# Performance work log

Hardware: AMD Instinct MI355X
Metric: run time of the kernel (lower is better)

## Reference

```python
import jax, jax.numpy as jnp
import numpy as np

EPS = 1e-8

def setup_inputs() -> dict:
    key = jax.random.key(0)
    ks = jax.random.split(key, 4)
    B, N, D = 16, 2048, 1024
    APP = 1024
    x = jax.random.normal(ks[0], (B, N, D), dtype=jnp.float32)
    mask = jax.random.uniform(ks[1], (N, B), dtype=jnp.float32)  # [N, B] per original
    Wp = jax.random.normal(ks[2], (1024, D), dtype=jnp.float32) * 0.02
    bp = jnp.zeros((1024,), dtype=jnp.float32)
    Wv = jax.random.normal(ks[3], (APP, D), dtype=jnp.float32) * 0.02
    bv = jnp.zeros((APP,), dtype=jnp.float32)
    return {"x": x, "mask": mask, "Wp": Wp, "bp": bp, "Wv": Wv, "bv": bv}

def reference(x, mask, Wp, bp, Wv, bv):
    # proj + ReLU: [B,N,1024]
    xp = jax.nn.relu(jnp.einsum('bnd,pd->bnp', x, Wp) + bp)
    # L2-normalize along feature dim (matches xp / (norm + eps))
    xp = xp / (jnp.linalg.norm(xp, axis=2, keepdims=True) + EPS)
    # mask: [N,B] -> [B,N] (transpose+reshape in original yields [B,1,N])
    m = mask.T  # [B, N]
    # att_i = sum_j m_j * <xp_i, xp_j> / sum_j m_j  == <xp_i, sum_j m_j xp_j> / sum_j m_j
    ws = jnp.einsum('bn,bnp->bp', m, xp)                # [B, 1024]
    att = jnp.einsum('bnp,bp->bn', xp, ws) / jnp.sum(m, axis=1, keepdims=True)  # [B, N]
    # value + ReLU: [B,N,APP]
    xv = jax.nn.relu(jnp.einsum('bnd,ad->bna', x, Wv) + bv)
    return att[:, :, None] * xv
```

## Files before the change

### kernel.cpp

```cpp
#include <hip/hip_runtime.h>

#define B_  16
#define N_  2048
#define D_  1024
#define P_  1024
#define M_  (B_*N_)

typedef __attribute__((ext_vector_type(8))) short bf16x8;
typedef __attribute__((ext_vector_type(4))) float f32x4;

__device__ __forceinline__ float bf2f(unsigned short u) {
    union { unsigned int i; float f; } v; v.i = ((unsigned int)u) << 16; return v.f;
}
__device__ __forceinline__ unsigned short f2bf(float f) {
    union { unsigned int i; float f; } v; v.f = f;
    unsigned int i = v.i;
    return (unsigned short)((i + 0x7FFFu + ((i >> 16) & 1u)) >> 16);
}

__device__ __forceinline__ void async_cp16(const void* g, void* s) {
    __builtin_amdgcn_global_load_lds((const __attribute__((address_space(1))) void*)g,
                                     (__attribute__((address_space(3))) void*)s,
                                     16, 0, 0);
}

__global__ void cvt_all_k(const float* __restrict__ x,  unsigned short* __restrict__ xb,
                          const float* __restrict__ Wp, unsigned short* __restrict__ Wpb,
                          const float* __restrict__ Wv, unsigned short* __restrict__ Wvb)
{
    const int stride = gridDim.x * 256 * 4;
    const int base = (blockIdx.x * 256 + threadIdx.x) * 4;
    for (int i = base; i < M_ * D_; i += stride) {
        float4 v = *(const float4*)(x + i);
        union { unsigned short u[4]; unsigned long long ll; } p;
        p.u[0]=f2bf(v.x); p.u[1]=f2bf(v.y); p.u[2]=f2bf(v.z); p.u[3]=f2bf(v.w);
        *(unsigned long long*)(xb + i) = p.ll;
    }
    for (int i = base; i < P_ * D_; i += stride) {
        float4 v = *(const float4*)(Wp + i);
        union { unsigned short u[4]; unsigned long long ll; } p;
        p.u[0]=f2bf(v.x); p.u[1]=f2bf(v.y); p.u[2]=f2bf(v.z); p.u[3]=f2bf(v.w);
        *(unsigned long long*)(Wpb + i) = p.ll;
    }
    for (int i = base; i < P_ * D_; i += stride) {
        float4 v = *(const float4*)(Wv + i);
        union { unsigned short u[4]; unsigned long long ll; } p;
        p.u[0]=f2bf(v.x); p.u[1]=f2bf(v.y); p.u[2]=f2bf(v.z); p.u[3]=f2bf(v.w);
        *(unsigned long long*)(Wvb + i) = p.ll;
    }
}

template<int MODE>
__global__ __launch_bounds__(512, 2) void gemm8p(const unsigned short* __restrict__ A,
                                                 const unsigned short* __restrict__ W,
                                                 const float* __restrict__ bias,
                                                 const float* __restrict__ att,
                                                 void* __restrict__ Cv)
{
    __shared__ unsigned short smem[65536];

    const int id  = blockIdx.x;
    const int xcd = id & 7, idx = id >> 3;
    const int bx  = idx & 3;
    const int by  = xcd * 16 + (idx >> 2);
    const int m0  = by << 8, p0 = bx << 8;

    const int t    = threadIdx.x;
    const int lane = t & 63, wave = t >> 6;
    const int wr   = wave >> 2, wc = wave & 3;
    const int lr   = lane & 15, lq = lane >> 4;

    const int aBase = (wr * 64 + lr) * 64;
    const int bBase = (wc * 32 + lr) * 64;
    const int c0 = ((lq       ^ (lr & 7)) & 7) * 8;
    const int c1 = (((lq | 4) ^ (lr & 7)) & 7) * 8;

    const int srowT = t >> 3;
    const int slot8 = (t & 7) * 8;
    const int lch8  = (((t & 7) ^ (srowT & 7)) & 7) * 8;
    const unsigned short* Ag = A + ((size_t)m0 << 10) + lch8;
    const unsigned short* Bg = W + ((size_t)p0 << 10) + lch8;

    auto stageA = [&](int buf, int rb, int tt) {
        const unsigned short* s = Ag + ((size_t)(rb + srowT) << 10) + (tt << 6);
        async_cp16(s,                      smem + buf * 16384 + (rb + srowT) * 64 + slot8);
        async_cp16(s + ((size_t)64 << 10), smem + buf * 16384 + (rb + 64 + srowT) * 64 + slot8);
    };
    auto stageB = [&](int buf, int rb, int tt) {
        const unsigned short* s = Bg + ((size_t)(rb + srowT) << 10) + (tt << 6);
        async_cp16(s,                      smem + 32768 + buf * 16384 + (rb + srowT) * 64 + slot8);
        async_cp16(s + ((size_t)64 << 10), smem + 32768 + buf * 16384 + (rb + 64 + srowT) * 64 + slot8);
    };

    f32x4 acc[8][4];
    #pragma unroll
    for (int i = 0; i < 8; ++i)
        #pragma unroll
        for (int j = 0; j < 4; ++j) acc[i][j] = (f32x4){0.f, 0.f, 0.f, 0.f};

    bf16x8 aR[2][4][2];
    bf16x8 bR[2][2];

    stageA(0, 0, 0); stageA(0, 128, 0); stageB(0, 0, 0); stageB(0, 128, 0);
    stageA(1, 0, 1); stageA(1, 128, 1); stageB(1, 0, 1); stageB(1, 128, 1);
    asm volatile("s_waitcnt vmcnt(8)" ::: "memory");
    __builtin_amdgcn_sched_barrier(0);
    __builtin_amdgcn_s_barrier();

#define VMW4 do { asm volatile("s_waitcnt vmcnt(4)" ::: "memory"); \
                  __builtin_amdgcn_sched_barrier(0); } while (0)
#define NOVM ((void)0)
#define PHASE(BUFC, MH, NH, RD_A, RD_B, STAGE_STMT, DO_VM) do {                       \
    if (RD_A) {                                                                       \
        const unsigned short* Ab_ = smem + (BUFC) * 16384 + (MH) * 8192 + aBase;      \
        _Pragma("unroll")                                                             \
        for (int i_ = 0; i_ < 4; ++i_) {                                              \
            aR[MH][i_][0] = *(const bf16x8*)(Ab_ + i_ * 1024 + c0);                   \
            aR[MH][i_][1] = *(const bf16x8*)(Ab_ + i_ * 1024 + c1);                   \
        }                                                                             \
    }                                                                                 \
    if (RD_B) {                                                                       \
        const unsigned short* Bb_ = smem + 32768 + (BUFC) * 16384 + (NH) * 8192 + bBase; \
        _Pragma("unroll")                                                             \
        for (int j_ = 0; j_ < 2; ++j_) {                                              \
            bR[j_][0] = *(const bf16x8*)(Bb_ + j_ * 1024 + c0);                       \
            bR[j_][1] = *(const bf16x8*)(Bb_ + j_ * 1024 + c1);                       \
        }                                                                             \
    }                                                                                 \
    STAGE_STMT;                                                                       \
    __builtin_amdgcn_s_barrier();                                                     \
    asm volatile("s_waitcnt lgkmcnt(0)" ::: "memory");                                \
    __builtin_amdgcn_sched_barrier(0);                                                \
    __builtin_amdgcn_s_setprio(1);                                                    \
    _Pragma("unroll")                                                                 \
    for (int h_ = 0; h_ < 2; ++h_)                                                    \
        _Pragma("unroll")                                                             \
        for (int i_ = 0; i_ < 4; ++i_)                                                \
            _Pragma("unroll")                                                         \
            for (int j_ = 0; j_ < 2; ++j_)                                            \
                acc[(MH) * 4 + i_][(NH) * 2 + j_] =                                   \
                    __builtin_amdgcn_mfma_f32_16x16x32_bf16(                          \
                        aR[MH][i_][h_], bR[j_][h_],                                   \
                        acc[(MH) * 4 + i_][(NH) * 2 + j_], 0, 0, 0);                  \
    __builtin_amdgcn_s_setprio(0);                                                    \
    DO_VM;                                                                            \
    __builtin_amdgcn_s_barrier();                                                     \
} while (0)

    #pragma unroll 1
    for (int it = 0; it < 8; ++it) {
        const int t1 = 2 * it + 1;
        const int t2 = (2 * it + 2) & 15;
        const int t3 = (2 * it + 3) & 15;
        PHASE(0, 0, 0, 1, 1, { if (it) stageA(1, 128, t1); }, NOVM);
        PHASE(0, 1, 0, 1, 0, { if (it) stageB(1, 128, t1); }, NOVM);
        PHASE(0, 1, 1, 0, 1, stageB(0, 0,   t2), NOVM);
        PHASE(0, 0, 1, 0, 0, stageA(0, 0,   t2), VMW4);
        PHASE(1, 0, 0, 1, 1, stageA(0, 128, t2), NOVM);
        PHASE(1, 1, 0, 1, 0, stageB(0, 128, t2), NOVM);
        PHASE(1, 1, 1, 0, 1, stageB(1, 0,   t3), NOVM);
        PHASE(1, 0, 1, 0, 0, stageA(1, 0,   t3), VMW4);
    }
#undef PHASE
#undef VMW4
#undef NOVM

    asm volatile("s_waitcnt vmcnt(0)" ::: "memory");
    __syncthreads();

    if (MODE == 0) {
        float bi[4];
        #pragma unroll
        for (int nj = 0; nj < 4; ++nj)
            bi[nj] = bias[p0 + ((nj >> 1) << 7) + wc * 32 + ((nj & 1) << 4) + lr];
        unsigned short* Cp = (unsigned short*)Cv;
        #pragma unroll
        for (int mh = 0; mh < 2; ++mh) {
            #pragma unroll
            for (int i = 0; i < 4; ++i) {
                const int rl = wr * 64 + i * 16 + lq * 4;
                #pragma unroll
                for (int nj = 0; nj < 4; ++nj) {
                    const int colL = ((nj >> 1) << 7) + wc * 32 + ((nj & 1) << 4) + lr;
                    #pragma unroll
                    for (int v = 0; v < 4; ++v) {
                        const float val = fmaxf(acc[mh * 4 + i][nj][v] + bi[nj], 0.f);
                        smem[(rl + v) * 256 + colL] = f2bf(val);
                    }
                }
            }
            __syncthreads();
            #pragma unroll
            for (int pas = 0; pas < 8; ++pas) {
                const int ix = pas * 512 + t;
                const int row = ix >> 5, ch = ix & 31;
                bf16x8 vv = *(const bf16x8*)(smem + row * 256 + ch * 8);
                *(bf16x8*)(Cp + (size_t)(m0 + mh * 128 + row) * P_ + p0 + ch * 8) = vv;
            }
            __syncthreads();
        }
    } else {
        float* Cp = (float*)Cv;
        #pragma unroll
        for (int mi = 0; mi < 8; ++mi) {
            const int row = m0 + ((mi >> 2) << 7) + wr * 64 + ((mi & 3) << 4) + lq * 4;
            float av[4];
            #pragma unroll
            for (int v = 0; v < 4; ++v) av[v] = att[row + v];
            #pragma unroll
            for (int nj = 0; nj < 4; ++nj) {
                const int col = p0 + ((nj >> 1) << 7) + wc * 32 + ((nj & 1) << 4) + lr;
                const float b0v = bias[col];
                #pragma unroll
                for (int v = 0; v < 4; ++v) {
                    const float val = fmaxf(acc[mi][nj][v] + b0v, 0.f);
                    Cp[(size_t)(row + v) * P_ + col] = val * av[v];
                }
            }
        }
    }
}

template<int MODE>
__global__ __launch_bounds__(256) void gemm_f32(const float* __restrict__ A,
                                                const float* __restrict__ W,
                                                const float* __restrict__ bias,
                                                const float* __restrict__ att,
                                                void* __restrict__ Cv)
{
    const int K = D_, BK = 32;
    __shared__ float As[128 * 32];
    __shared__ float Bs[128 * 32];
    const int id = blockIdx.x;
    const int bx = (id >> 3) & 7;
    const int by = ((id >> 6) << 3) | (id & 7);
    const int m0 = by * 128, p0 = bx * 128;
    const int wave = threadIdx.x >> 6, lane = threadIdx.x & 63;
    const int wr = wave >> 1, wc = wave & 1;
    const int srow = wave * 32 + (lane >> 3);
    const int scol = (lane & 7) * 4;
    const float* ag = A + (size_t)(m0 + srow) * K + scol;
    const float* bg = W + (size_t)(p0 + srow) * K + scol;
    float* as = &As[srow * BK + scol];
    float* bs = &Bs[srow * BK + scol];
    f32x4 acc[4][4];
    #pragma unroll
    for (int i = 0; i < 4; i++)
        #pragma unroll
        for (int j = 0; j < 4; j++) acc[i][j] = (f32x4){0.f,0.f,0.f,0.f};
    const int lr = lane & 15, lq = lane >> 4;
    const float* Ar = &As[(wr * 64 + lr) * BK + lq * 8];
    const float* Br = &Bs[(wc * 64 + lr) * BK + lq * 8];
    for (int kb = 0; kb < K; kb += BK) {
        #pragma unroll
        for (int s = 0; s < 4; s++) {
            async_cp16(ag + (size_t)s * 8 * K + kb, as + s * 8 * BK);
            async_cp16(bg + (size_t)s * 8 * K + kb, bs + s * 8 * BK);
        }
        __syncthreads();
        bf16x8 af[4], bf[4];
        #pragma unroll
        for (int i = 0; i < 4; i++) {
            f32x4 a0 = *(const f32x4*)(Ar + i * 16 * BK);
            f32x4 a1 = *(const f32x4*)(Ar + i * 16 * BK + 4);
            #pragma unroll
            for (int e = 0; e < 4; e++) {
                union { float f; unsigned int u; } c;
                c.f = a0[e]; af[i][e]     = (short)(c.u >> 16);
                c.f = a1[e]; af[i][e + 4] = (short)(c.u >> 16);
            }
        }
        #pragma unroll
        for (int j = 0; j < 4; j++) {
            f32x4 b0 = *(const f32x4*)(Br + j * 16 * BK);
            f32x4 b1 = *(const f32x4*)(Br + j * 16 * BK + 4);
            #pragma unroll
            for (int e = 0; e < 4; e++) {
                union { float f; unsigned int u; } c;
                c.f = b0[e]; bf[j][e]     = (short)(c.u >> 16);
                c.f = b1[e]; bf[j][e + 4] = (short)(c.u >> 16);
            }
        }
        #pragma unroll
        for (int i = 0; i < 4; i++)
            #pragma unroll
            for (int j = 0; j < 4; j++)
                acc[i][j] = __builtin_amdgcn_mfma_f32_16x16x32_bf16(af[i], bf[j], acc[i][j], 0, 0, 0);
        __syncthreads();
    }
    const int crow0 = m0 + wr * 64 + lq * 4;
    const int ccol0 = p0 + wc * 64 + lr;
    #pragma unroll
    for (int i = 0; i < 4; i++) {
        float attv[4];
        if (MODE == 1) {
            #pragma unroll
            for (int v = 0; v < 4; v++) attv[v] = att[crow0 + i * 16 + v];
        }
        #pragma unroll
        for (int j = 0; j < 4; j++) {
            const int col = ccol0 + j * 16;
            const float bi = bias[col];
            #pragma unroll
            for (int v = 0; v < 4; v++) {
                const int row = crow0 + i * 16 + v;
                float val = fmaxf(acc[i][j][v] + bi, 0.0f);
                if (MODE == 0) ((unsigned short*)Cv)[(size_t)row * P_ + col] = f2bf(val);
                else           ((float*)Cv)[(size_t)row * P_ + col] = val * attv[v];
            }
        }
    }
}

__global__ __launch_bounds__(256) void fused_nc_k(const unsigned short* __restrict__ X1,
                                                  const float* __restrict__ mask,
                                                  float* __restrict__ inv,
                                                  float* __restrict__ wsv,
                                                  float* __restrict__ msum)
{
    __shared__ float accw[4][1024];
    __shared__ float mred[4];
    const int b = blockIdx.y, nc = blockIdx.x;
    const int wave = threadIdx.x >> 6, lane = threadIdx.x & 63;
    float acc[16];
    #pragma unroll
    for (int e = 0; e < 16; e++) acc[e] = 0.f;
    float msub = 0.f;
    const int rbase = b * N_ + nc * 32 + wave * 8;
    const int nbase = nc * 32 + wave * 8;
    for (int t = 0; t < 8; t++) {
        const int r = rbase + t;
        const unsigned short* row = X1 + (size_t)r * P_;
        bf16x8 u0 = *(const bf16x8*)(row + lane * 16);
        bf16x8 u1 = *(const bf16x8*)(row + lane * 16 + 8);
        float v[16], s = 0.f;
        #pragma unroll
        for (int e = 0; e < 8; e++) { v[e] = bf2f((unsigned short)u0[e]); s += v[e]*v[e]; }
        #pragma unroll
        for (int e = 0; e < 8; e++) { v[8+e] = bf2f((unsigned short)u1[e]); s += v[8+e]*v[8+e]; }
        #pragma unroll
        for (int off = 32; off > 0; off >>= 1) s += __shfl_down(s, off);
        s = __shfl(s, 0);
        const float iv = 1.f / (sqrtf(s) + 1e-8f);
        const float mk = mask[(nbase + t) * B_ + b];
        if (lane == 0) { inv[r] = iv; msub += mk; }
        const float w = mk * iv;
        #pragma unroll
        for (int e = 0; e < 16; e++) acc[e] += w * v[e];
    }
    #pragma unroll
    for (int e = 0; e < 16; e++) accw[wave][e * 64 + lane] = acc[e];
    if (lane == 0) mred[wave] = msub;
    __syncthreads();
    #pragma unroll
    for (int q = 0; q < 4; q++) {
        const int p = threadIdx.x * 4 + q;
        const int col = (p & 63) * 16 + (p >> 6);
        float ssum = accw[0][p] + accw[1][p] + accw[2][p] + accw[3][p];
        atomicAdd(&wsv[b * P_ + col], ssum);
    }
    if (threadIdx.x == 0) atomicAdd(&msum[b], mred[0] + mred[1] + mred[2] + mred[3]);
}

__global__ void att_k(const unsigned short* __restrict__ X1,
                      const float* __restrict__ wsvec,
                      const float* __restrict__ inv,
                      const float* __restrict__ msum,
                      float* __restrict__ att)
{
    const int r = blockIdx.x * 4 + (threadIdx.x >> 6);
    const int lane = threadIdx.x & 63;
    const int b = r >> 11;
    const unsigned short* row = X1 + (size_t)r * P_;
    const float* w = wsvec + b * P_;
    bf16x8 u0 = *(const bf16x8*)(row + lane * 8);
    bf16x8 u1 = *(const bf16x8*)(row + 512 + lane * 8);
    f32x4 w0 = *(const f32x4*)(w + lane * 8);
    f32x4 w1 = *(const f32x4*)(w + lane * 8 + 4);
    f32x4 w2 = *(const f32x4*)(w + 512 + lane * 8);
    f32x4 w3 = *(const f32x4*)(w + 512 + lane * 8 + 4);
    float s = 0.f;
    #pragma unroll
    for (int k = 0; k < 4; k++) s += bf2f((unsigned short)u0[k]) * w0[k];
    #pragma unroll
    for (int k = 0; k < 4; k++) s += bf2f((unsigned short)u0[k + 4]) * w1[k];
    #pragma unroll
    for (int k = 0; k < 4; k++) s += bf2f((unsigned short)u1[k]) * w2[k];
    #pragma unroll
    for (int k = 0; k < 4; k++) s += bf2f((unsigned short)u1[k + 4]) * w3[k];
    #pragma unroll
    for (int off = 32; off > 0; off >>= 1) s += __shfl_down(s, off);
    if (lane == 0) att[r] = s * inv[r] / msum[b];
}

extern "C" void kernel_launch(void* const* d_in, const int* in_sizes, int n_in,
                              void* d_out, int out_size, void* d_ws, size_t ws_size,
                              hipStream_t stream)
{
    const float* x    = (const float*)d_in[0];
    const float* mask = (const float*)d_in[1];
    const float* Wp   = (const float*)d_in[2];
    const float* bp   = (const float*)d_in[3];
    const float* Wv   = (const float*)d_in[4];
    const float* bv   = (const float*)d_in[5];
    float* out = (float*)d_out;

    unsigned short* X1 = (unsigned short*)d_out;

    const size_t xb_bytes = (size_t)M_ * D_ * 2;
    const size_t wb_bytes = (size_t)P_ * D_ * 2;
    const size_t f_bytes  = 2 * (size_t)M_ * 4 + (size_t)B_ * P_ * 4 + 64;
    const bool big_ws = ws_size >= xb_bytes + 2 * wb_bytes + f_bytes;

    char* ws = (char*)d_ws;
    size_t off = 0;
    unsigned short *xb = nullptr, *Wpb = nullptr, *Wvb = nullptr;
    if (big_ws) {
        xb  = (unsigned short*)(ws + off); off += xb_bytes;
        Wpb = (unsigned short*)(ws + off); off += wb_bytes;
        Wvb = (unsigned short*)(ws + off); off += wb_bytes;
    }
    float* inv  = (float*)(ws + off); off += (size_t)M_ * 4;
    float* att  = (float*)(ws + off); off += (size_t)M_ * 4;
    float* wsv  = (float*)(ws + off); off += (size_t)B_ * P_ * 4;
    float* msum = (float*)(ws + off); off += 64;

    hipMemsetAsync(wsv, 0, (size_t)B_ * P_ * 4 + 64, stream);

    if (big_ws) {
        cvt_all_k<<<2048, 256, 0, stream>>>(x, xb, Wp, Wpb, Wv, Wvb);
        gemm8p<0><<<512, 512, 0, stream>>>(xb, Wpb, bp, nullptr, X1);
    } else {
        const int gblocks = (P_ / 128) * (M_ / 128);
        gemm_f32<0><<<gblocks, 256, 0, stream>>>(x, Wp, bp, nullptr, X1);
    }
    fused_nc_k<<<dim3(64, B_), 256, 0, stream>>>(X1, mask, inv, wsv, msum);
    att_k<<<M_ / 4, 256, 0, stream>>>(X1, wsv, inv, msum, att);
    if (big_ws) gemm8p<1><<<512, 512, 0, stream>>>(xb, Wvb, bv, att, out);
    else {
        const int gblocks = (P_ / 128) * (M_ / 128);
        gemm_f32<1><<<gblocks, 256, 0, stream>>>(x, Wv, bv, att, out);
    }
}
```

Baseline: 410.2 us.

## Software-pipeline LDS fragment reads ahead of MFMA phases with finer waitcnts

Restructures the GEMM main loop so LDS reads for the next sub-tile are issued before the current MFMA block. Partial lgkmcnt waits replace full drains, and B fragments are double-buffered per N-half. The goal is to hide LDS latency behind matrix math instead of stalling on lgkmcnt(0) each phase. This costs extra registers for the duplicated B fragments, and the hand-counted vmcnt/lgkmcnt values must match the issue order exactly.

```diff
diff --git a/kernel.cpp b/kernel.cpp
--- a/kernel.cpp
+++ b/kernel.cpp
@@ -99,38 +99,25 @@
         for (int j = 0; j < 4; ++j) acc[i][j] = (f32x4){0.f, 0.f, 0.f, 0.f};
 
     bf16x8 aR[2][4][2];
-    bf16x8 bR[2][2];
-
-    stageA(0, 0, 0); stageA(0, 128, 0); stageB(0, 0, 0); stageB(0, 128, 0);
-    stageA(1, 0, 1); stageA(1, 128, 1); stageB(1, 0, 1); stageB(1, 128, 1);
-    asm volatile("s_waitcnt vmcnt(8)" ::: "memory");
-    __builtin_amdgcn_sched_barrier(0);
-    __builtin_amdgcn_s_barrier();
-
-#define VMW4 do { asm volatile("s_waitcnt vmcnt(4)" ::: "memory"); \
-                  __builtin_amdgcn_sched_barrier(0); } while (0)
-#define NOVM ((void)0)
-#define PHASE(BUFC, MH, NH, RD_A, RD_B, STAGE_STMT, DO_VM) do {                       \
-    if (RD_A) {                                                                       \
-        const unsigned short* Ab_ = smem + (BUFC) * 16384 + (MH) * 8192 + aBase;      \
-        _Pragma("unroll")                                                             \
-        for (int i_ = 0; i_ < 4; ++i_) {                                              \
-            aR[MH][i_][0] = *(const bf16x8*)(Ab_ + i_ * 1024 + c0);                   \
-            aR[MH][i_][1] = *(const bf16x8*)(Ab_ + i_ * 1024 + c1);                   \
-        }                                                                             \
-    }                                                                                 \
-    if (RD_B) {                                                                       \
-        const unsigned short* Bb_ = smem + 32768 + (BUFC) * 16384 + (NH) * 8192 + bBase; \
-        _Pragma("unroll")                                                             \
-        for (int j_ = 0; j_ < 2; ++j_) {                                              \
-            bR[j_][0] = *(const bf16x8*)(Bb_ + j_ * 1024 + c0);                       \
-            bR[j_][1] = *(const bf16x8*)(Bb_ + j_ * 1024 + c1);                       \
-        }                                                                             \
-    }                                                                                 \
-    STAGE_STMT;                                                                       \
-    __builtin_amdgcn_s_barrier();                                                     \
-    asm volatile("s_waitcnt lgkmcnt(0)" ::: "memory");                                \
-    __builtin_amdgcn_sched_barrier(0);                                                \
+    bf16x8 bR[2][2][2];
+
+#define RD_A(BUF, MH) do {                                                            \
+    const unsigned short* Ab_ = smem + (BUF) * 16384 + (MH) * 8192 + aBase;           \
+    _Pragma("unroll")                                                                 \
+    for (int i_ = 0; i_ < 4; ++i_) {                                                  \
+        aR[MH][i_][0] = *(const bf16x8*)(Ab_ + i_ * 1024 + c0);                       \
+        aR[MH][i_][1] = *(const bf16x8*)(Ab_ + i_ * 1024 + c1);                       \
+    } } while (0)
+
+#define RD_B(BUF, NH) do {                                                            \
+    const unsigned short* Bb_ = smem + 32768 + (BUF) * 16384 + (NH) * 8192 + bBase;   \
+    _Pragma("unroll")                                                                 \
+    for (int j_ = 0; j_ < 2; ++j_) {                                                  \
+        bR[NH][j_][0] = *(const bf16x8*)(Bb_ + j_ * 1024 + c0);                       \
+        bR[NH][j_][1] = *(const bf16x8*)(Bb_ + j_ * 1024 + c1);                       \
+    } } while (0)
+
+#define MM(MH, NH) do {                                                               \
     __builtin_amdgcn_s_setprio(1);                                                    \
     _Pragma("unroll")                                                                 \
     for (int h_ = 0; h_ < 2; ++h_)                                                    \
@@ -140,32 +127,57 @@
             for (int j_ = 0; j_ < 2; ++j_)                                            \
                 acc[(MH) * 4 + i_][(NH) * 2 + j_] =                                   \
                     __builtin_amdgcn_mfma_f32_16x16x32_bf16(                          \
-                        aR[MH][i_][h_], bR[j_][h_],                                   \
+                        aR[MH][i_][h_], bR[NH][j_][h_],                               \
                         acc[(MH) * 4 + i_][(NH) * 2 + j_], 0, 0, 0);                  \
-    __builtin_amdgcn_s_setprio(0);                                                    \
-    DO_VM;                                                                            \
-    __builtin_amdgcn_s_barrier();                                                     \
-} while (0)
+    __builtin_amdgcn_s_setprio(0); } while (0)
+
+#define LGKM(N) do { asm volatile("s_waitcnt lgkmcnt(" #N ")" ::: "memory");          \
+                     __builtin_amdgcn_sched_barrier(0); } while (0)
+#define VMC(N)  do { asm volatile("s_waitcnt vmcnt(" #N ")" ::: "memory");            \
+                     __builtin_amdgcn_sched_barrier(0); } while (0)
+#define BAR()   __builtin_amdgcn_s_barrier()
+
+    stageA(0, 0, 0); stageB(0, 0, 0); stageA(0, 128, 0); stageB(0, 128, 0);
+    stageA(1, 0, 1); stageB(1, 0, 1); stageA(1, 128, 1); stageB(1, 128, 1);
+    VMC(8);
+    BAR();
+    RD_A(0, 0);
+    RD_B(0, 0);
 
     #pragma unroll 1
     for (int it = 0; it < 8; ++it) {
         const int t1 = 2 * it + 1;
         const int t2 = (2 * it + 2) & 15;
         const int t3 = (2 * it + 3) & 15;
-        PHASE(0, 0, 0, 1, 1, { if (it) stageA(1, 128, t1); }, NOVM);
-        PHASE(0, 1, 0, 1, 0, { if (it) stageB(1, 128, t1); }, NOVM);
-        PHASE(0, 1, 1, 0, 1, stageB(0, 0,   t2), NOVM);
-        PHASE(0, 0, 1, 0, 0, stageA(0, 0,   t2), VMW4);
-        PHASE(1, 0, 0, 1, 1, stageA(0, 128, t2), NOVM);
-        PHASE(1, 1, 0, 1, 0, stageB(0, 128, t2), NOVM);
-        PHASE(1, 1, 1, 0, 1, stageB(1, 0,   t3), NOVM);
-        PHASE(1, 0, 1, 0, 0, stageA(1, 0,   t3), VMW4);
-    }
-#undef PHASE
-#undef VMW4
-#undef NOVM
-
-    asm volatile("s_waitcnt vmcnt(0)" ::: "memory");
+        RD_A(0, 1); stageB(1, 128, t1);
+        BAR(); LGKM(8); MM(0, 0); BAR();
+        RD_B(0, 1); stageA(1, 128, t1);
+        BAR(); LGKM(4); MM(1, 0); BAR();
+        stageA(0, 0, t2);
+        BAR(); LGKM(0); MM(1, 1); VMC(6); BAR();
+        stageB(0, 0, t2);
+        BAR(); LGKM(0); MM(0, 1);
+        RD_A(1, 0); RD_B(1, 0);
+        VMC(4); BAR();
+        RD_A(1, 1); stageB(0, 128, t2);
+        BAR(); LGKM(8); MM(0, 0); BAR();
+        RD_B(1, 1); stageA(0, 128, t2);
+        BAR(); LGKM(4); MM(1, 0); BAR();
+        stageA(1, 0, t3);
+        BAR(); LGKM(0); MM(1, 1); VMC(6); BAR();
+        stageB(1, 0, t3);
+        BAR(); LGKM(0); MM(0, 1);
+        RD_A(0, 0); RD_B(0, 0);
+        VMC(4); BAR();
+    }
+#undef RD_A
+#undef RD_B
+#undef MM
+#undef LGKM
+#undef VMC
+#undef BAR
+
+    asm volatile("s_waitcnt vmcnt(0) lgkmcnt(0)" ::: "memory");
     __syncthreads();
 
     if (MODE == 0) {
```

Result: no change. 414.2 us (+1.0%).
